# Optimization experiments

Hardware: AMD Instinct MI355X
Metric: run time of the kernel (lower is better)

The kernel has to match this reference:

```python
import jax, jax.numpy as jnp
import numpy as np

N_NODES = 50000
N_EDGES = 1_600_000
IN_CH = 128
HIDDEN = 64
OUT_CH = 1


def glorot(key, shape):
    limit = np.sqrt(6.0 / (shape[0] + shape[1]))
    return jax.random.uniform(key, shape, jnp.float32, -limit, limit)


def setup_inputs() -> dict:
    key = jax.random.key(0)
    ks = jax.random.split(key, 6)
    x = jax.random.normal(ks[0], (N_NODES, IN_CH), jnp.float32)
    edge_index = jax.random.randint(ks[1], (2, N_EDGES), 0, N_NODES, jnp.int64)
    W1 = glorot(ks[2], (IN_CH, HIDDEN))
    b1 = jnp.zeros((HIDDEN,), jnp.float32)
    W2 = glorot(ks[3], (HIDDEN, HIDDEN // 2))
    b2 = jnp.zeros((HIDDEN // 2,), jnp.float32)
    Wh = glorot(ks[4], (HIDDEN // 2, OUT_CH))
    bh = jnp.zeros((OUT_CH,), jnp.float32)
    return {"x": x, "edge_index": edge_index, "W1": W1, "b1": b1,
            "W2": W2, "b2": b2, "Wh": Wh, "bh": bh}


def gcn_conv(x, src, dst, W, b):
    """PyG-style GCNConv: H' = D^{-1/2} (A + I) D^{-1/2} X W + b."""
    n = x.shape[0]
    h = x @ W  # transform first (smaller message dim)
    # degree of A + I (all edge weights = 1, self-loop weight = 1)
    deg = jax.ops.segment_sum(jnp.ones(src.shape[0], h.dtype), dst,
                              num_segments=n) + 1.0
    dinv = deg ** -0.5
    norm = dinv[src] * dinv[dst]                      # [E]
    msg = h[src] * norm[:, None]                      # [E, F] gather
    agg = jax.ops.segment_sum(msg, dst, num_segments=n)  # scatter-add
    agg = agg + h * (dinv * dinv)[:, None]            # self-loop term
    return agg + b


def reference(x, edge_index, W1, b1, W2, b2, Wh, bh):
    src, dst = edge_index[0], edge_index[1]
    h = jax.nn.relu(gcn_conv(x, src, dst, W1, b1))
    # dropout: inference mode (training=False) -> identity
    h = jax.nn.relu(gcn_conv(h, src, dst, W2, b2))
    return h @ Wh + bh
```

## Files before the change

### kernel.cpp

```cpp
#include <hip/hip_runtime.h>

#define N_NODES 50000
#define IN_CH 128
#define HID 64
#define HID2 32

constexpr int NB = 391;
constexpr int CHUNK = 4096;
constexpr int CAP = 5120;
#define FPSCALE 524288.0f
#define FPINV   0x1p-19f

__device__ __forceinline__ unsigned short f2bf(float f) {
    union { float f; unsigned u; } v; v.f = f;
    unsigned r = v.u + 0x7fff + ((v.u >> 16) & 1);
    return (unsigned short)(r >> 16);
}
__device__ __forceinline__ float bflo(unsigned d) {
    union { unsigned u; float f; } v; v.u = d << 16; return v.f;
}
__device__ __forceinline__ float bfhi(unsigned d) {
    union { unsigned u; float f; } v; v.u = d & 0xffff0000u; return v.f;
}

__global__ __launch_bounds__(1024) void bin_kernel(const int* __restrict__ src,
                                                   const int* __restrict__ dst,
                                                   int* __restrict__ bcur,
                                                   unsigned short* __restrict__ psrc,
                                                   unsigned char* __restrict__ pbyte, int E) {
    __shared__ int hist[NB], lbase[NB], gbase[NB], lcur[NB];
    __shared__ unsigned outp[CHUNK];
    int tid = threadIdx.x;
    int base = blockIdx.x * CHUNK;
    int cnt = min(CHUNK, E - base);
    for (int i = tid; i < NB; i += 1024) hist[i] = 0;
    int es[CHUNK / 1024], ed[CHUNK / 1024];
    __syncthreads();
#pragma unroll
    for (int k = 0; k < CHUNK / 1024; k++) {
        int e = base + k * 1024 + tid;
        if (e < E) {
            es[k] = src[e];
            ed[k] = dst[e];
            atomicAdd(&hist[ed[k] >> 7], 1);
        }
    }
    __syncthreads();
    if (tid == 0) {
        int run = 0;
        for (int b = 0; b < NB; b++) { int t = hist[b]; lbase[b] = run; run += t; }
    }
    __syncthreads();
    for (int i = tid; i < NB; i += 1024) {
        gbase[i] = i * CAP + (hist[i] ? atomicAdd(&bcur[i], hist[i]) : 0);
        lcur[i] = lbase[i];
    }
    __syncthreads();
#pragma unroll
    for (int k = 0; k < CHUNK / 1024; k++) {
        int e = base + k * 1024 + tid;
        if (e < E) {
            int b = ed[k] >> 7;
            int p = atomicAdd(&lcur[b], 1);
            outp[p] = ((unsigned)es[k] << 16) | (unsigned)ed[k];
        }
    }
    __syncthreads();
#pragma unroll
    for (int k = 0; k < CHUNK / 1024; k++) {
        int i = k * 1024 + tid;
        if (i < cnt) {
            unsigned p = outp[i];
            int d = (int)(p & 0xffffu);
            int b = d >> 7;
            int gp = gbase[b] + (i - lbase[b]);
            psrc[gp] = (unsigned short)(p >> 16);
            pbyte[gp] = (unsigned char)(d & 127);
        }
    }
}

__global__ __launch_bounds__(1024) void fine_kernel(unsigned short* __restrict__ psrc,
                                                    const unsigned char* __restrict__ pbyte,
                                                    const int* __restrict__ bcur,
                                                    int* __restrict__ off,
                                                    unsigned short* __restrict__ len,
                                                    float* __restrict__ dinv, int N) {
    __shared__ unsigned short lsrc[CAP];
    __shared__ unsigned char lb[CAP];
    __shared__ int fh[128], fb[128], fc[128];
    int b = blockIdx.x, tid = threadIdx.x;
    int gb = b * CAP;
    int cnt = min(bcur[b], CAP);
    if (tid < 128) fh[tid] = 0;
    __syncthreads();
    for (int i = tid; i < cnt; i += 1024) {
        lsrc[i] = psrc[gb + i];
        int dl = pbyte[gb + i];
        lb[i] = (unsigned char)dl;
        atomicAdd(&fh[dl], 1);
    }
    __syncthreads();
    if (tid == 0) {
        int run = 0;
        for (int j = 0; j < 128; j++) { int t = fh[j]; fb[j] = run; run += t; }
    }
    __syncthreads();
    if (tid < 128) {
        fc[tid] = fb[tid];
        int node = (b << 7) + tid;
        if (node < N) {
            off[node] = gb + fb[tid];
            len[node] = (unsigned short)fh[tid];
            dinv[node] = rsqrtf((float)fh[tid] + 1.0f);
        }
    }
    __syncthreads();
    for (int i = tid; i < cnt; i += 1024) {
        int p = atomicAdd(&fc[lb[i]], 1);
        psrc[gb + p] = lsrc[i];
    }
}

template <int K, int J, int NPB>
__global__ __launch_bounds__(256) void gemm_s_kernel(const float* __restrict__ X,
                                                     const float* __restrict__ W,
                                                     const float* __restrict__ dinv,
                                                     unsigned short* __restrict__ out, int N) {
    constexpr int QJ = J / 4;
    constexpr int NPT = NPB / (256 / QJ);
    static_assert(NPT == 2, "layout assumes 2 nodes/thread");
    constexpr int RG = K / 4;
    constexpr int RS = K + 4;
    __shared__ float Ws[K * J];
    __shared__ float Xs[NPB * RS];
    int tid = threadIdx.x;
    for (int i = tid; i < K * J / 4; i += 256) ((float4*)Ws)[i] = ((const float4*)W)[i];
    int n0 = blockIdx.x * NPB;
    for (int i = tid; i < NPB * RG; i += 256) {
        int r = i / RG, c = i % RG;
        int n = n0 + r;
        float4 v = make_float4(0.f, 0.f, 0.f, 0.f);
        if (n < N) v = ((const float4*)(X + (size_t)n * K))[c];
        *(float4*)&Xs[r * RS + ((c ^ (r & 7)) << 2)] = v;
    }
    __syncthreads();
    int q = tid % QJ, g = (tid / QJ) * NPT;
    const float* xr0 = &Xs[g * RS];
    const float* xr1 = &Xs[(g + 1) * RS];
    int sw0 = g & 7, sw1 = (g + 1) & 7;
    float4 a0 = make_float4(0.f, 0.f, 0.f, 0.f);
    float4 a1 = make_float4(0.f, 0.f, 0.f, 0.f);
#pragma unroll 8
    for (int k = 0; k < K; k++) {
        float4 w = *(const float4*)&Ws[k * J + q * 4];
        float x0 = xr0[(((k >> 2) ^ sw0) << 2) + (k & 3)];
        float x1 = xr1[(((k >> 2) ^ sw1) << 2) + (k & 3)];
        a0.x += x0 * w.x; a0.y += x0 * w.y; a0.z += x0 * w.z; a0.w += x0 * w.w;
        a1.x += x1 * w.x; a1.y += x1 * w.y; a1.z += x1 * w.z; a1.w += x1 * w.w;
    }
    int n = n0 + g;
    if (n < N) {
        float d0 = dinv[n] * FPSCALE;
        ushort4 o = make_ushort4(f2bf(a0.x * d0), f2bf(a0.y * d0),
                                 f2bf(a0.z * d0), f2bf(a0.w * d0));
        *(ushort4*)(out + (size_t)n * J + q * 4) = o;
    }
    if (n + 1 < N) {
        float d1 = dinv[n + 1] * FPSCALE;
        ushort4 o = make_ushort4(f2bf(a1.x * d1), f2bf(a1.y * d1),
                                 f2bf(a1.z * d1), f2bf(a1.w * d1));
        *(ushort4*)(out + (size_t)(n + 1) * J + q * 4) = o;
    }
}

__global__ __launch_bounds__(256) void agg1_fused_kernel(const unsigned short* __restrict__ sorted_src,
                                                         const int* __restrict__ off,
                                                         const unsigned short* __restrict__ len,
                                                         const float* __restrict__ dinv,
                                                         const unsigned short* __restrict__ xws,
                                                         const float* __restrict__ b1,
                                                         const float* __restrict__ W2,
                                                         unsigned short* __restrict__ hws, int N) {
    __shared__ float hrow[4][HID];
    int tid = threadIdx.x, wid = tid >> 6, lane = tid & 63;
    int n = blockIdx.x * 4 + wid;
    if (n >= N) return;
    int g = lane >> 3, fl = lane & 7;
    int start = off[n], end = start + len[n];
    int acc[8] = {0, 0, 0, 0, 0, 0, 0, 0};
    int i = start + g;
    for (; i + 8 < end; i += 16) {
        int s0 = sorted_src[i], s1 = sorted_src[i + 8];
        uint4 q0 = *(const uint4*)(xws + (size_t)s0 * HID + fl * 8);
        uint4 q1 = *(const uint4*)(xws + (size_t)s1 * HID + fl * 8);
        acc[0] += (int)bflo(q0.x) + (int)bflo(q1.x);
        acc[1] += (int)bfhi(q0.x) + (int)bfhi(q1.x);
        acc[2] += (int)bflo(q0.y) + (int)bflo(q1.y);
        acc[3] += (int)bfhi(q0.y) + (int)bfhi(q1.y);
        acc[4] += (int)bflo(q0.z) + (int)bflo(q1.z);
        acc[5] += (int)bfhi(q0.z) + (int)bfhi(q1.z);
        acc[6] += (int)bflo(q0.w) + (int)bflo(q1.w);
        acc[7] += (int)bfhi(q0.w) + (int)bfhi(q1.w);
    }
    if (i < end) {
        int s = sorted_src[i];
        uint4 q = *(const uint4*)(xws + (size_t)s * HID + fl * 8);
        acc[0] += (int)bflo(q.x); acc[1] += (int)bfhi(q.x);
        acc[2] += (int)bflo(q.y); acc[3] += (int)bfhi(q.y);
        acc[4] += (int)bflo(q.z); acc[5] += (int)bfhi(q.z);
        acc[6] += (int)bflo(q.w); acc[7] += (int)bfhi(q.w);
    }
#pragma unroll
    for (int m = 8; m <= 32; m <<= 1)
#pragma unroll
        for (int j = 0; j < 8; j++) acc[j] += __shfl_xor(acc[j], m, 64);
    if (g == 0) {
        float dis = dinv[n] * FPINV;
        uint4 q = *(const uint4*)(xws + (size_t)n * HID + fl * 8);
        int sv[8] = {(int)bflo(q.x), (int)bfhi(q.x), (int)bflo(q.y), (int)bfhi(q.y),
                     (int)bflo(q.z), (int)bfhi(q.z), (int)bflo(q.w), (int)bfhi(q.w)};
        float4 bb0 = *(const float4*)(b1 + fl * 8);
        float4 bb1 = *(const float4*)(b1 + fl * 8 + 4);
        float bbv[8] = {bb0.x, bb0.y, bb0.z, bb0.w, bb1.x, bb1.y, bb1.z, bb1.w};
        float o[8];
#pragma unroll
        for (int j = 0; j < 8; j++)
            o[j] = fmaxf((float)(acc[j] + sv[j]) * dis + bbv[j], 0.f);
        *(float4*)&hrow[wid][fl * 8]     = make_float4(o[0], o[1], o[2], o[3]);
        *(float4*)&hrow[wid][fl * 8 + 4] = make_float4(o[4], o[5], o[6], o[7]);
    }
    int j = lane & 31;
    float p = 0.f;
#pragma unroll 8
    for (int k = 0; k < HID; k++)
        p += hrow[wid][k] * W2[k * HID2 + j];
    if (lane < 32)
        hws[(size_t)n * HID2 + j] = f2bf(p * dinv[n] * FPSCALE);
}

__global__ __launch_bounds__(256) void agg2_final_kernel(const unsigned short* __restrict__ sorted_src,
                                                         const int* __restrict__ off,
                                                         const unsigned short* __restrict__ len,
                                                         const float* __restrict__ dinv,
                                                         const unsigned short* __restrict__ hws,
                                                         const float* __restrict__ b2,
                                                         const float* __restrict__ Wh,
                                                         const float* __restrict__ bh,
                                                         float* __restrict__ out, int N) {
    int lane = threadIdx.x & 63;
    int n = blockIdx.x * 4 + (threadIdx.x >> 6);
    if (n >= N) return;
    int g = lane >> 2, fl = lane & 3;
    int start = off[n], end = start + len[n];
    int acc[8] = {0, 0, 0, 0, 0, 0, 0, 0};
    int i = start + g;
    for (; i + 16 < end; i += 32) {
        int s0 = sorted_src[i], s1 = sorted_src[i + 16];
        uint4 q0 = *(const uint4*)(hws + (size_t)s0 * HID2 + fl * 8);
        uint4 q1 = *(const uint4*)(hws + (size_t)s1 * HID2 + fl * 8);
        acc[0] += (int)bflo(q0.x) + (int)bflo(q1.x);
        acc[1] += (int)bfhi(q0.x) + (int)bfhi(q1.x);
        acc[2] += (int)bflo(q0.y) + (int)bflo(q1.y);
        acc[3] += (int)bfhi(q0.y) + (int)bfhi(q1.y);
        acc[4] += (int)bflo(q0.z) + (int)bflo(q1.z);
        acc[5] += (int)bfhi(q0.z) + (int)bfhi(q1.z);
        acc[6] += (int)bflo(q0.w) + (int)bflo(q1.w);
        acc[7] += (int)bfhi(q0.w) + (int)bfhi(q1.w);
    }
    if (i < end) {
        int s = sorted_src[i];
        uint4 q = *(const uint4*)(hws + (size_t)s * HID2 + fl * 8);
        acc[0] += (int)bflo(q.x); acc[1] += (int)bfhi(q.x);
        acc[2] += (int)bflo(q.y); acc[3] += (int)bfhi(q.y);
        acc[4] += (int)bflo(q.z); acc[5] += (int)bfhi(q.z);
        acc[6] += (int)bflo(q.w); acc[7] += (int)bfhi(q.w);
    }
#pragma unroll
    for (int m = 4; m <= 32; m <<= 1)
#pragma unroll
        for (int j = 0; j < 8; j++) acc[j] += __shfl_xor(acc[j], m, 64);
    float dis = dinv[n] * FPINV;
    uint4 q = *(const uint4*)(hws + (size_t)n * HID2 + fl * 8);
    int sv[8] = {(int)bflo(q.x), (int)bfhi(q.x), (int)bflo(q.y), (int)bfhi(q.y),
                 (int)bflo(q.z), (int)bfhi(q.z), (int)bflo(q.w), (int)bfhi(q.w)};
    float4 bb0 = *(const float4*)(b2 + fl * 8);
    float4 bb1 = *(const float4*)(b2 + fl * 8 + 4);
    float bbv[8] = {bb0.x, bb0.y, bb0.z, bb0.w, bb1.x, bb1.y, bb1.z, bb1.w};
    float4 wv0 = *(const float4*)(Wh + fl * 8);
    float4 wv1 = *(const float4*)(Wh + fl * 8 + 4);
    float wvv[8] = {wv0.x, wv0.y, wv0.z, wv0.w, wv1.x, wv1.y, wv1.z, wv1.w};
    float p = 0.f;
#pragma unroll
    for (int j = 0; j < 8; j++)
        p += fmaxf((float)(acc[j] + sv[j]) * dis + bbv[j], 0.f) * wvv[j];
    p += __shfl_xor(p, 1, 64);
    p += __shfl_xor(p, 2, 64);
    if (lane == 0) out[n] = p + bh[0];
}

extern "C" void kernel_launch(void* const* d_in, const int* in_sizes, int n_in,
                              void* d_out, int out_size, void* d_ws, size_t ws_size,
                              hipStream_t stream) {
    const float* x  = (const float*)d_in[0];
    const int*   ei = (const int*)d_in[1];
    const float* W1 = (const float*)d_in[2];
    const float* b1 = (const float*)d_in[3];
    const float* W2 = (const float*)d_in[4];
    const float* b2 = (const float*)d_in[5];
    const float* Wh = (const float*)d_in[6];
    const float* bh = (const float*)d_in[7];
    float* out = (float*)d_out;

    const int N = N_NODES;
    const int E = in_sizes[1] / 2;
    const int* src = ei;
    const int* dst = ei + E;

    int* ws = (int*)d_ws;
    int*            bcur  = ws;
    int*            off   = bcur + 512;
    unsigned short* len   = (unsigned short*)(off + 50048);
    float*          dinv  = (float*)((int*)len + 25024);
    unsigned short* psrc  = (unsigned short*)(dinv + 50048);
    unsigned char*  pbyte = (unsigned char*)(psrc + (size_t)NB * CAP);
    unsigned short* xws   = (unsigned short*)(pbyte + (size_t)NB * CAP);
    unsigned short* hws   = xws + (size_t)N * HID;

    hipMemsetAsync(bcur, 0, NB * sizeof(int), stream);

    int eblocks = (E + CHUNK - 1) / CHUNK;
    bin_kernel<<<eblocks, 1024, 0, stream>>>(src, dst, bcur, psrc, pbyte, E);
    fine_kernel<<<NB, 1024, 0, stream>>>(psrc, pbyte, bcur, off, len, dinv, N);

    gemm_s_kernel<IN_CH, HID, 32><<<(N + 31) / 32, 256, 0, stream>>>(x, W1, dinv, xws, N);
    agg1_fused_kernel<<<(N + 3) / 4, 256, 0, stream>>>(psrc, off, len, dinv, xws, b1, W2, hws, N);
    agg2_final_kernel<<<(N + 3) / 4, 256, 0, stream>>>(psrc, off, len, dinv, hws, b2, Wh, bh, out, N);
}
```

Baseline: 213.1 us.

## Store layer-1 features as int16 fixed point and preload neighbor indices via shuffles

The layer-1 GEMM output is quantized to clamped int16 fixed point with a smaller scale instead of bf16, so the aggregation can sign-extend and integer-add directly without a bf16-to-float-to-int conversion. Both aggregation kernels also get a fast path for nodes with 64 or fewer edges: the wave loads all neighbor indices in one coalesced read and broadcasts them with shuffles, which removes dependent index loads from the gather loop. The int16 format trades dynamic range for precision and clamps large values, which could cost accuracy. The general path now handles one edge per iteration, a small unroll reduction.

```diff
diff --git a/kernel.cpp b/kernel.cpp
--- a/kernel.cpp
+++ b/kernel.cpp
@@ -10,6 +10,8 @@
 constexpr int CAP = 5120;
 #define FPSCALE 524288.0f
 #define FPINV   0x1p-19f
+#define T1SCALE 2048.0f
+#define T1INV   0x1p-11f
 
 __device__ __forceinline__ unsigned short f2bf(float f) {
     union { float f; unsigned u; } v; v.f = f;
@@ -21,6 +23,13 @@
 }
 __device__ __forceinline__ float bfhi(unsigned d) {
     union { unsigned u; float f; } v; v.u = d & 0xffff0000u; return v.f;
+}
+__device__ __forceinline__ void acc2(int& a0, int& a1, unsigned u) {
+    a0 += (int)(short)(u & 0xffffu);
+    a1 += ((int)u) >> 16;
+}
+__device__ __forceinline__ unsigned pack16(int a, int b) {
+    return ((unsigned)a & 0xffffu) | ((unsigned)b << 16);
 }
 
 __global__ __launch_bounds__(1024) void bin_kernel(const int* __restrict__ src,
@@ -126,7 +135,7 @@
 __global__ __launch_bounds__(256) void gemm_s_kernel(const float* __restrict__ X,
                                                      const float* __restrict__ W,
                                                      const float* __restrict__ dinv,
-                                                     unsigned short* __restrict__ out, int N) {
+                                                     short* __restrict__ out, int N) {
     constexpr int QJ = J / 4;
     constexpr int NPT = NPB / (256 / QJ);
     static_assert(NPT == 2, "layout assumes 2 nodes/thread");
@@ -159,18 +168,18 @@
         a0.x += x0 * w.x; a0.y += x0 * w.y; a0.z += x0 * w.z; a0.w += x0 * w.w;
         a1.x += x1 * w.x; a1.y += x1 * w.y; a1.z += x1 * w.z; a1.w += x1 * w.w;
     }
-    int n = n0 + g;
-    if (n < N) {
-        float d0 = dinv[n] * FPSCALE;
-        ushort4 o = make_ushort4(f2bf(a0.x * d0), f2bf(a0.y * d0),
-                                 f2bf(a0.z * d0), f2bf(a0.w * d0));
-        *(ushort4*)(out + (size_t)n * J + q * 4) = o;
-    }
-    if (n + 1 < N) {
-        float d1 = dinv[n + 1] * FPSCALE;
-        ushort4 o = make_ushort4(f2bf(a1.x * d1), f2bf(a1.y * d1),
-                                 f2bf(a1.z * d1), f2bf(a1.w * d1));
-        *(ushort4*)(out + (size_t)(n + 1) * J + q * 4) = o;
+#pragma unroll
+    for (int t = 0; t < NPT; t++) {
+        int n = n0 + g + t;
+        if (n < N) {
+            float4 a = t ? a1 : a0;
+            float d0 = dinv[n] * T1SCALE;
+            int v0 = max(-32767, min(32767, (int)lrintf(a.x * d0)));
+            int v1 = max(-32767, min(32767, (int)lrintf(a.y * d0)));
+            int v2 = max(-32767, min(32767, (int)lrintf(a.z * d0)));
+            int v3 = max(-32767, min(32767, (int)lrintf(a.w * d0)));
+            *(uint2*)(out + (size_t)n * J + q * 4) = make_uint2(pack16(v0, v1), pack16(v2, v3));
+        }
     }
 }
 
@@ -178,7 +187,7 @@
                                                          const int* __restrict__ off,
                                                          const unsigned short* __restrict__ len,
                                                          const float* __restrict__ dinv,
-                                                         const unsigned short* __restrict__ xws,
+                                                         const short* __restrict__ xtab,
                                                          const float* __restrict__ b1,
                                                          const float* __restrict__ W2,
                                                          unsigned short* __restrict__ hws, int N) {
@@ -187,39 +196,47 @@
     int n = blockIdx.x * 4 + wid;
     if (n >= N) return;
     int g = lane >> 3, fl = lane & 7;
-    int start = off[n], end = start + len[n];
+    int start = off[n], len_ = len[n];
+    const unsigned* tb = (const unsigned*)xtab;
     int acc[8] = {0, 0, 0, 0, 0, 0, 0, 0};
-    int i = start + g;
-    for (; i + 8 < end; i += 16) {
-        int s0 = sorted_src[i], s1 = sorted_src[i + 8];
-        uint4 q0 = *(const uint4*)(xws + (size_t)s0 * HID + fl * 8);
-        uint4 q1 = *(const uint4*)(xws + (size_t)s1 * HID + fl * 8);
-        acc[0] += (int)bflo(q0.x) + (int)bflo(q1.x);
-        acc[1] += (int)bfhi(q0.x) + (int)bfhi(q1.x);
-        acc[2] += (int)bflo(q0.y) + (int)bflo(q1.y);
-        acc[3] += (int)bfhi(q0.y) + (int)bfhi(q1.y);
-        acc[4] += (int)bflo(q0.z) + (int)bflo(q1.z);
-        acc[5] += (int)bfhi(q0.z) + (int)bfhi(q1.z);
-        acc[6] += (int)bflo(q0.w) + (int)bflo(q1.w);
-        acc[7] += (int)bfhi(q0.w) + (int)bfhi(q1.w);
-    }
-    if (i < end) {
-        int s = sorted_src[i];
-        uint4 q = *(const uint4*)(xws + (size_t)s * HID + fl * 8);
-        acc[0] += (int)bflo(q.x); acc[1] += (int)bfhi(q.x);
-        acc[2] += (int)bflo(q.y); acc[3] += (int)bfhi(q.y);
-        acc[4] += (int)bflo(q.z); acc[5] += (int)bfhi(q.z);
-        acc[6] += (int)bflo(q.w); acc[7] += (int)bfhi(q.w);
+    if (len_ <= 64) {
+        int sall = (lane < len_) ? (int)sorted_src[start + lane] : 0;
+        int nit = (len_ + 15) >> 4;
+        for (int t = 0; t < nit; t++) {
+            int e0 = g + (t << 4), e1 = e0 + 8;
+            bool l0 = e0 < len_, l1 = e1 < len_;
+            int s0 = __shfl(sall, l0 ? e0 : 0, 64);
+            int s1 = __shfl(sall, l1 ? e1 : 0, 64);
+            uint4 q0 = *(const uint4*)(tb + (size_t)s0 * 32 + fl * 4);
+            uint4 q1 = *(const uint4*)(tb + (size_t)s1 * 32 + fl * 4);
+            if (!l0) q0 = make_uint4(0, 0, 0, 0);
+            if (!l1) q1 = make_uint4(0, 0, 0, 0);
+            acc2(acc[0], acc[1], q0.x); acc2(acc[2], acc[3], q0.y);
+            acc2(acc[4], acc[5], q0.z); acc2(acc[6], acc[7], q0.w);
+            acc2(acc[0], acc[1], q1.x); acc2(acc[2], acc[3], q1.y);
+            acc2(acc[4], acc[5], q1.z); acc2(acc[6], acc[7], q1.w);
+        }
+    } else {
+        int i = start + g, end = start + len_;
+        for (; i < end; i += 8) {
+            int s = sorted_src[i];
+            uint4 q = *(const uint4*)(tb + (size_t)s * 32 + fl * 4);
+            acc2(acc[0], acc[1], q.x); acc2(acc[2], acc[3], q.y);
+            acc2(acc[4], acc[5], q.z); acc2(acc[6], acc[7], q.w);
+        }
     }
 #pragma unroll
     for (int m = 8; m <= 32; m <<= 1)
 #pragma unroll
         for (int j = 0; j < 8; j++) acc[j] += __shfl_xor(acc[j], m, 64);
     if (g == 0) {
-        float dis = dinv[n] * FPINV;
-        uint4 q = *(const uint4*)(xws + (size_t)n * HID + fl * 8);
-        int sv[8] = {(int)bflo(q.x), (int)bfhi(q.x), (int)bflo(q.y), (int)bfhi(q.y),
-                     (int)bflo(q.z), (int)bfhi(q.z), (int)bflo(q.w), (int)bfhi(q.w)};
+        float dis = dinv[n] * T1INV;
+        uint4 q = *(const uint4*)(tb + (size_t)n * 32 + fl * 4);
+        int sv[8];
+        sv[0] = (int)(short)(q.x & 0xffffu); sv[1] = ((int)q.x) >> 16;
+        sv[2] = (int)(short)(q.y & 0xffffu); sv[3] = ((int)q.y) >> 16;
+        sv[4] = (int)(short)(q.z & 0xffffu); sv[5] = ((int)q.z) >> 16;
+        sv[6] = (int)(short)(q.w & 0xffffu); sv[7] = ((int)q.w) >> 16;
         float4 bb0 = *(const float4*)(b1 + fl * 8);
         float4 bb1 = *(const float4*)(b1 + fl * 8 + 4);
         float bbv[8] = {bb0.x, bb0.y, bb0.z, bb0.w, bb1.x, bb1.y, bb1.z, bb1.w};
@@ -252,29 +269,39 @@
     int n = blockIdx.x * 4 + (threadIdx.x >> 6);
     if (n >= N) return;
     int g = lane >> 2, fl = lane & 3;
-    int start = off[n], end = start + len[n];
+    int start = off[n], len_ = len[n];
     int acc[8] = {0, 0, 0, 0, 0, 0, 0, 0};
-    int i = start + g;
-    for (; i + 16 < end; i += 32) {
-        int s0 = sorted_src[i], s1 = sorted_src[i + 16];
-        uint4 q0 = *(const uint4*)(hws + (size_t)s0 * HID2 + fl * 8);
-        uint4 q1 = *(const uint4*)(hws + (size_t)s1 * HID2 + fl * 8);
-        acc[0] += (int)bflo(q0.x) + (int)bflo(q1.x);
-        acc[1] += (int)bfhi(q0.x) + (int)bfhi(q1.x);
-        acc[2] += (int)bflo(q0.y) + (int)bflo(q1.y);
-        acc[3] += (int)bfhi(q0.y) + (int)bfhi(q1.y);
-        acc[4] += (int)bflo(q0.z) + (int)bflo(q1.z);
-        acc[5] += (int)bfhi(q0.z) + (int)bfhi(q1.z);
-        acc[6] += (int)bflo(q0.w) + (int)bflo(q1.w);
-        acc[7] += (int)bfhi(q0.w) + (int)bfhi(q1.w);
-    }
-    if (i < end) {
-        int s = sorted_src[i];
-        uint4 q = *(const uint4*)(hws + (size_t)s * HID2 + fl * 8);
-        acc[0] += (int)bflo(q.x); acc[1] += (int)bfhi(q.x);
-        acc[2] += (int)bflo(q.y); acc[3] += (int)bfhi(q.y);
-        acc[4] += (int)bflo(q.z); acc[5] += (int)bfhi(q.z);
-        acc[6] += (int)bflo(q.w); acc[7] += (int)bfhi(q.w);
+    if (len_ <= 64) {
+        int sall = (lane < len_) ? (int)sorted_src[start + lane] : 0;
+        int nit = (len_ + 31) >> 5;
+        for (int t = 0; t < nit; t++) {
+            int e0 = g + (t << 5), e1 = e0 + 16;
+            bool l0 = e0 < len_, l1 = e1 < len_;
+            int s0 = __shfl(sall, l0 ? e0 : 0, 64);
+            int s1 = __shfl(sall, l1 ? e1 : 0, 64);
+            uint4 q0 = *(const uint4*)(hws + (size_t)s0 * HID2 + fl * 8);
+            uint4 q1 = *(const uint4*)(hws + (size_t)s1 * HID2 + fl * 8);
+            if (!l0) q0 = make_uint4(0, 0, 0, 0);
+            if (!l1) q1 = make_uint4(0, 0, 0, 0);
+            acc[0] += (int)bflo(q0.x) + (int)bflo(q1.x);
+            acc[1] += (int)bfhi(q0.x) + (int)bfhi(q1.x);
+            acc[2] += (int)bflo(q0.y) + (int)bflo(q1.y);
+            acc[3] += (int)bfhi(q0.y) + (int)bfhi(q1.y);
+            acc[4] += (int)bflo(q0.z) + (int)bflo(q1.z);
+            acc[5] += (int)bfhi(q0.z) + (int)bfhi(q1.z);
+            acc[6] += (int)bflo(q0.w) + (int)bflo(q1.w);
+            acc[7] += (int)bfhi(q0.w) + (int)bfhi(q1.w);
+        }
+    } else {
+        int i = start + g, end = start + len_;
+        for (; i < end; i += 16) {
+            int s = sorted_src[i];
+            uint4 q = *(const uint4*)(hws + (size_t)s * HID2 + fl * 8);
+            acc[0] += (int)bflo(q.x); acc[1] += (int)bfhi(q.x);
+            acc[2] += (int)bflo(q.y); acc[3] += (int)bfhi(q.y);
+            acc[4] += (int)bflo(q.z); acc[5] += (int)bfhi(q.z);
+            acc[6] += (int)bflo(q.w); acc[7] += (int)bfhi(q.w);
+        }
     }
 #pragma unroll
     for (int m = 4; m <= 32; m <<= 1)
@@ -324,8 +351,8 @@
     float*          dinv  = (float*)((int*)len + 25024);
     unsigned short* psrc  = (unsigned short*)(dinv + 50048);
     unsigned char*  pbyte = (unsigned char*)(psrc + (size_t)NB * CAP);
-    unsigned short* xws   = (unsigned short*)(pbyte + (size_t)NB * CAP);
-    unsigned short* hws   = xws + (size_t)N * HID;
+    short*          xtab  = (short*)(pbyte + (size_t)NB * CAP);
+    unsigned short* hws   = (unsigned short*)(xtab + (size_t)N * HID);
 
     hipMemsetAsync(bcur, 0, NB * sizeof(int), stream);
 
@@ -333,7 +360,7 @@
     bin_kernel<<<eblocks, 1024, 0, stream>>>(src, dst, bcur, psrc, pbyte, E);
     fine_kernel<<<NB, 1024, 0, stream>>>(psrc, pbyte, bcur, off, len, dinv, N);
 
-    gemm_s_kernel<IN_CH, HID, 32><<<(N + 31) / 32, 256, 0, stream>>>(x, W1, dinv, xws, N);
-    agg1_fused_kernel<<<(N + 3) / 4, 256, 0, stream>>>(psrc, off, len, dinv, xws, b1, W2, hws, N);
+    gemm_s_kernel<IN_CH, HID, 32><<<(N + 31) / 32, 256, 0, stream>>>(x, W1, dinv, xtab, N);
+    agg1_fused_kernel<<<(N + 3) / 4, 256, 0, stream>>>(psrc, off, len, dinv, xtab, b1, W2, hws, N);
     agg2_final_kernel<<<(N + 3) / 4, 256, 0, stream>>>(psrc, off, len, dinv, hws, b2, Wh, bh, out, N);
 }
```

After: 207.8 us. -2.5%, faster.
